# Optimization experiments

Measured on AMD Instinct MI355X. Metric: run time of the kernel, lower is better.

Reference implementation:

```python
import jax, jax.numpy as jnp
import numpy as np

BATCH, IN_WIDTH, OUT_FEATURES, FAN_IN = 512, 4096, 4096, 128

def setup_inputs() -> dict:
    key = jax.random.key(0)
    k1, k2, k3, k4 = jax.random.split(key, 4)
    input = jax.random.normal(k1, (BATCH, IN_WIDTH), dtype=jnp.float32)
    weight = jax.random.normal(k2, (OUT_FEATURES, FAN_IN), dtype=jnp.float32)
    bias = jax.random.normal(k3, (OUT_FEATURES,), dtype=jnp.float32)
    indx_seqs = jax.random.randint(k4, (OUT_FEATURES, FAN_IN), 0, IN_WIDTH, dtype=jnp.int64)
    return {"input": input, "weight": weight, "bias": bias, "indx_seqs": indx_seqs}

def reference(input, weight, bias, indx_seqs):
    # gather: (B, out_features, fan_in)
    gathered = input[:, indx_seqs]
    # elementwise mul with weight (out_features, fan_in), reduce over fan_in
    return jnp.einsum('bof,of->bo', gathered, weight) + bias
```

## Files before the change

### kernel.cpp

```cpp
#include <hip/hip_runtime.h>
#include <hip/hip_bf16.h>

#define BATCH    512
#define IN_WIDTH 4096
#define OUT_F    4096
#define FAN_IN   128
#define BCHUNK   16
#define NBG      (BATCH / BCHUNK)
#define OBLK     512
#define NOG      (OUT_F / OBLK)

typedef float    v2f __attribute__((ext_vector_type(2)));
typedef uint32_t v4u __attribute__((ext_vector_type(4)));

__global__ __launch_bounds__(256) void k_prep(const float* __restrict__ in,
                                              const int* __restrict__ idx,
                                              const float* __restrict__ weight,
                                              uint16_t* __restrict__ inTg,
                                              uint2* __restrict__ pk) {
  __shared__ float tile[32][33];
  const int blk = blockIdx.x;
  const int t   = threadIdx.x;
  if (blk < 2048) {
    const int jt = (blk & 127) * 32;
    const int bt = (blk >> 7) * 32;
    const int tx = t & 31;
    const int ty = t >> 5;
#pragma unroll
    for (int r = 0; r < 32; r += 8) {
      tile[ty + r][tx] = in[(size_t)(bt + ty + r) * IN_WIDTH + (jt + tx)];
    }
    __syncthreads();
#pragma unroll
    for (int r = 0; r < 32; r += 8) {
      const int b = bt + tx;
      const int j = jt + ty + r;
      __hip_bfloat16 hv = __float2bfloat16(tile[tx][ty + r]);
      inTg[((size_t)(b >> 4) * IN_WIDTH + j) * BCHUNK + (b & 15)] =
          *reinterpret_cast<const uint16_t*>(&hv);
    }
  } else {
    const int i = (blk - 2048) * 256 + t;
    uint2 e;
    e.x = (uint32_t)idx[i];
    e.y = __float_as_uint(weight[i]);
    pk[i] = e;
  }
}

__global__ __launch_bounds__(1024, 4) void k_gather_lds(const uint16_t* __restrict__ inTg,
                                                        const uint2* __restrict__ pk,
                                                        const float* __restrict__ bias,
                                                        float* __restrict__ out) {
  extern __shared__ char lds[];
  const int og = blockIdx.x;
  const int bg = blockIdx.y;
  const int t  = threadIdx.x;

  {
    const v4u* __restrict__ src =
        reinterpret_cast<const v4u*>(inTg + (size_t)bg * IN_WIDTH * BCHUNK);
#pragma unroll
    for (int i = 0; i < 8; ++i) {
      const v4u* g = src + i * 1024 + t;
      char* d = lds + ((t >> 6) << 10) + (i << 14);
      __builtin_amdgcn_global_load_lds(
          (const __attribute__((address_space(1))) void*)g,
          (__attribute__((address_space(3))) void*)d, 16, 0, 0);
    }
    asm volatile("s_waitcnt vmcnt(0)" ::: "memory");
  }
  __syncthreads();

  const int wv = t >> 6;
  const int l  = t & 63;
  const int o  = og * OBLK + wv * 32 + (l >> 1);
  const int p  = l & 1;

  const uint32_t sb = (uint32_t)(size_t)lds + (uint32_t)(p * 16);

  const uint4* __restrict__ pko =
      reinterpret_cast<const uint4*>(pk + (size_t)o * FAN_IN);

  v2f a0 = {0.f, 0.f}, a1 = {0.f, 0.f}, a2 = {0.f, 0.f}, a3 = {0.f, 0.f};

#define DSREAD(d, jj) \
  asm volatile("ds_read_b128 %0, %1" : "=v"(d) : "v"(sb + ((jj) << 5)))

#define WAIT4() do { asm volatile("s_waitcnt lgkmcnt(4)" ::: "memory"); \
                     __builtin_amdgcn_sched_barrier(0); } while (0)
#define WAIT0() do { asm volatile("s_waitcnt lgkmcnt(0)" ::: "memory"); \
                     __builtin_amdgcn_sched_barrier(0); } while (0)

#define CONSUME(v, wbits)                                              \
  do {                                                                 \
    const float wf_ = __uint_as_float(wbits);                          \
    v2f w2_; w2_[0] = wf_; w2_[1] = wf_;                               \
    v2f x0_, x1_, x2_, x3_;                                            \
    x0_[0] = __uint_as_float((v)[0] << 16);                            \
    x0_[1] = __uint_as_float((v)[0] & 0xffff0000u);                    \
    x1_[0] = __uint_as_float((v)[1] << 16);                            \
    x1_[1] = __uint_as_float((v)[1] & 0xffff0000u);                    \
    x2_[0] = __uint_as_float((v)[2] << 16);                            \
    x2_[1] = __uint_as_float((v)[2] & 0xffff0000u);                    \
    x3_[0] = __uint_as_float((v)[3] << 16);                            \
    x3_[1] = __uint_as_float((v)[3] & 0xffff0000u);                    \
    a0 += x0_ * w2_; a1 += x1_ * w2_; a2 += x2_ * w2_; a3 += x3_ * w2_;\
  } while (0)

  uint4 q0a = pko[0], q0b = pko[1];
  uint4 q1a = pko[2], q1b = pko[3];
  uint4 q2a = pko[4], q2b = pko[5];
  uint4 q3a = pko[6], q3b = pko[7];

  v4u vA0, vA1, vA2, vA3, vB0, vB1, vB2, vB3;
  uint32_t wA0, wA1, wA2, wA3, wB0, wB1, wB2, wB3;

  DSREAD(vA0, q0a.x); DSREAD(vA1, q0a.z); DSREAD(vA2, q0b.x); DSREAD(vA3, q0b.z);
  wA0 = q0a.y; wA1 = q0a.w; wA2 = q0b.y; wA3 = q0b.w;

#define STEP(Cc, QI0, QI1, QR0, QR1,                                   \
             VC0, VC1, VC2, VC3, WC0, WC1, WC2, WC3,                   \
             VI0, VI1, VI2, VI3, WI0, WI1, WI2, WI3)                   \
  do {                                                                 \
    DSREAD(VI0, QI0.x); DSREAD(VI1, QI0.z);                            \
    DSREAD(VI2, QI1.x); DSREAD(VI3, QI1.z);                            \
    WI0 = QI0.y; WI1 = QI0.w; WI2 = QI1.y; WI3 = QI1.w;                \
    {                                                                  \
      const int gn_ = ((Cc) + 4 > 31) ? 31 : ((Cc) + 4);               \
      QR0 = pko[2 * gn_];                                              \
      QR1 = pko[2 * gn_ + 1];                                          \
    }                                                                  \
    WAIT4();                                                           \
    CONSUME(VC0, WC0); CONSUME(VC1, WC1);                              \
    CONSUME(VC2, WC2); CONSUME(VC3, WC3);                              \
  } while (0)

#define STEP_A(Cc, QI0, QI1, QR0, QR1)                                   \
  STEP(Cc, QI0, QI1, QR0, QR1,                                           \
       vA0, vA1, vA2, vA3, wA0, wA1, wA2, wA3,                           \
       vB0, vB1, vB2, vB3, wB0, wB1, wB2, wB3)
#define STEP_B(Cc, QI0, QI1, QR0, QR1)                                   \
  STEP(Cc, QI0, QI1, QR0, QR1,                                           \
       vB0, vB1, vB2, vB3, wB0, wB1, wB2, wB3,                           \
       vA0, vA1, vA2, vA3, wA0, wA1, wA2, wA3)

#pragma unroll 1
  for (int cb = 0; cb < 28; cb += 4) {
    STEP_A(cb + 0, q1a, q1b, q0a, q0b);
    STEP_B(cb + 1, q2a, q2b, q1a, q1b);
    STEP_A(cb + 2, q3a, q3b, q2a, q2b);
    STEP_B(cb + 3, q0a, q0b, q3a, q3b);
  }
  STEP_A(28, q1a, q1b, q0a, q0b);
  STEP_B(29, q2a, q2b, q1a, q1b);
  STEP_A(30, q3a, q3b, q2a, q2b);
  WAIT0();
  CONSUME(vB0, wB0); CONSUME(vB1, wB1); CONSUME(vB2, wB2); CONSUME(vB3, wB3);

  const float bz = bias[o];
  const float r[8] = {a0[0], a0[1], a1[0], a1[1], a2[0], a2[1], a3[0], a3[1]};
  const size_t obase = (size_t)(bg * BCHUNK + p * 8) * OUT_F + o;
#pragma unroll
  for (int i = 0; i < 8; ++i) out[obase + (size_t)i * OUT_F] = r[i] + bz;

#undef STEP_B
#undef STEP_A
#undef STEP
#undef CONSUME
#undef WAIT4
#undef WAIT0
#undef DSREAD
}

extern "C" void kernel_launch(void* const* d_in, const int* in_sizes, int n_in,
                              void* d_out, int out_size, void* d_ws, size_t ws_size,
                              hipStream_t stream) {
  const float* input  = (const float*)d_in[0];
  const float* weight = (const float*)d_in[1];
  const float* bias   = (const float*)d_in[2];
  const int*   idx    = (const int*)d_in[3];
  float* out = (float*)d_out;

  uint16_t* inTg = (uint16_t*)d_ws;
  uint2*    pk   = (uint2*)((char*)d_ws + 4u * 1024 * 1024);

  k_prep<<<dim3(4096), dim3(256), 0, stream>>>(input, idx, weight, inTg, pk);
  k_gather_lds<<<dim3(NOG, NBG), dim3(1024), IN_WIDTH * BCHUNK * 2, stream>>>(
      inTg, pk, bias, out);
}
```

Before: 35.89 us.

## Split staged input rows into padded even/odd halves to spread LDS banks

Changes the bf16 staged-input layout so even and odd input columns live in two halves of the per-batch-group slice. The odd half is offset by an extra 16 bytes, and the packed indices are pre-encoded to match. The goal is to change the LDS bank mapping of the random ds_read_b128 gathers and reduce bank conflicts. In exchange the LDS footprint grows slightly beyond 128 KiB, a single-thread tail copy is added, and the workspace offsets shift.

```diff
diff --git a/kernel.cpp b/kernel.cpp
--- a/kernel.cpp
+++ b/kernel.cpp
@@ -9,14 +9,20 @@
 #define NBG      (BATCH / BCHUNK)
 #define OBLK     512
 #define NOG      (OUT_F / OBLK)
+#define ODD_BASE 65552u
+#define SLICE_B  131088u
 
 typedef float    v2f __attribute__((ext_vector_type(2)));
 typedef uint32_t v4u __attribute__((ext_vector_type(4)));
+
+__device__ __forceinline__ uint32_t jenc(uint32_t j) {
+  return ((j >> 1) << 5) + (j & 1) * ODD_BASE;
+}
 
 __global__ __launch_bounds__(256) void k_prep(const float* __restrict__ in,
                                               const int* __restrict__ idx,
                                               const float* __restrict__ weight,
-                                              uint16_t* __restrict__ inTg,
+                                              char* __restrict__ inTg,
                                               uint2* __restrict__ pk) {
   __shared__ float tile[32][33];
   const int blk = blockIdx.x;
@@ -34,21 +40,22 @@
 #pragma unroll
     for (int r = 0; r < 32; r += 8) {
       const int b = bt + tx;
-      const int j = jt + ty + r;
+      const uint32_t j = jt + ty + r;
       __hip_bfloat16 hv = __float2bfloat16(tile[tx][ty + r]);
-      inTg[((size_t)(b >> 4) * IN_WIDTH + j) * BCHUNK + (b & 15)] =
+      *reinterpret_cast<uint16_t*>(
+          inTg + (size_t)(b >> 4) * SLICE_B + jenc(j) + (b & 15) * 2) =
           *reinterpret_cast<const uint16_t*>(&hv);
     }
   } else {
     const int i = (blk - 2048) * 256 + t;
     uint2 e;
-    e.x = (uint32_t)idx[i];
+    e.x = jenc((uint32_t)idx[i]);
     e.y = __float_as_uint(weight[i]);
     pk[i] = e;
   }
 }
 
-__global__ __launch_bounds__(1024, 4) void k_gather_lds(const uint16_t* __restrict__ inTg,
+__global__ __launch_bounds__(1024, 4) void k_gather_lds(const char* __restrict__ inTg,
                                                         const uint2* __restrict__ pk,
                                                         const float* __restrict__ bias,
                                                         float* __restrict__ out) {
@@ -58,16 +65,19 @@
   const int t  = threadIdx.x;
 
   {
-    const v4u* __restrict__ src =
-        reinterpret_cast<const v4u*>(inTg + (size_t)bg * IN_WIDTH * BCHUNK);
+    const char* src = inTg + (size_t)bg * SLICE_B;
 #pragma unroll
     for (int i = 0; i < 8; ++i) {
-      const v4u* g = src + i * 1024 + t;
+      const char* g = src + i * 16384 + t * 16;
       char* d = lds + ((t >> 6) << 10) + (i << 14);
       __builtin_amdgcn_global_load_lds(
           (const __attribute__((address_space(1))) void*)g,
           (__attribute__((address_space(3))) void*)d, 16, 0, 0);
     }
+    if (t == 0) {
+      const v4u tail = *reinterpret_cast<const v4u*>(src + (SLICE_B - 16));
+      *reinterpret_cast<v4u*>(lds + (SLICE_B - 16)) = tail;
+    }
     asm volatile("s_waitcnt vmcnt(0)" ::: "memory");
   }
   __syncthreads();
@@ -84,8 +94,8 @@
 
   v2f a0 = {0.f, 0.f}, a1 = {0.f, 0.f}, a2 = {0.f, 0.f}, a3 = {0.f, 0.f};
 
-#define DSREAD(d, jj) \
-  asm volatile("ds_read_b128 %0, %1" : "=v"(d) : "v"(sb + ((jj) << 5)))
+#define DSREAD(d, je) \
+  asm volatile("ds_read_b128 %0, %1" : "=v"(d) : "v"(sb + (je)))
 
 #define WAIT4() do { asm volatile("s_waitcnt lgkmcnt(4)" ::: "memory"); \
                      __builtin_amdgcn_sched_barrier(0); } while (0)
@@ -182,10 +192,9 @@
   const int*   idx    = (const int*)d_in[3];
   float* out = (float*)d_out;
 
-  uint16_t* inTg = (uint16_t*)d_ws;
-  uint2*    pk   = (uint2*)((char*)d_ws + 4u * 1024 * 1024);
+  char*  inTg = (char*)d_ws;
+  uint2* pk   = (uint2*)((char*)d_ws + 6u * 1024 * 1024);
 
   k_prep<<<dim3(4096), dim3(256), 0, stream>>>(input, idx, weight, inTg, pk);
-  k_gather_lds<<<dim3(NOG, NBG), dim3(1024), IN_WIDTH * BCHUNK * 2, stream>>>(
-      inTg, pk, bias, out);
-}
+  k_gather_lds<<<dim3(NOG, NBG), dim3(1024), SLICE_B, stream>>>(inTg, pk, bias, out);
+}
```

Result: no change. 36.02 us (+0.4%).
